# Kernel optimization log

Measured on AMD Instinct MI355X. Metric: run time of the kernel, lower is better.

The kernel has to match this reference:

```python
import jax, jax.numpy as jnp
import numpy as np

B, N, D = 8, 900, 256
SA_H, CA_H = 8, 8
L, P = 4, 4
FF = 2048
SHAPES = ((128, 128), (64, 64), (32, 32), (16, 16))
STARTS = (0, 16384, 20480, 21504)
S = 21760
D_BAND = (D // 6) * 2   # 84
D_ROPE = 3 * D_BAND     # 252
NF = D_BAND // 2        # 42
EPS = 1e-5


def _ln(x, g, b):
    mu = jnp.mean(x, -1, keepdims=True)
    var = jnp.mean((x - mu) ** 2, -1, keepdims=True)
    return (x - mu) * jax.lax.rsqrt(var + EPS) * g + b


def _rotate_half(x):
    x1 = x[..., 0::2]
    x2 = x[..., 1::2]
    return jnp.stack([-x2, x1], axis=-1).reshape(x.shape)


def _rope(q, k, boxes):
    freqs = 1.0 / (10000.0 ** (jnp.arange(NF, dtype=jnp.float32) / NF))
    cx, cy = boxes[..., 0], boxes[..., 1]
    xy = cx * cy

    def cs(v, f):
        a = v[..., None] * f
        return jnp.repeat(jnp.cos(a), 2, -1), jnp.repeat(jnp.sin(a), 2, -1)

    cx_c, cx_s = cs(cx, freqs)
    cy_c, cy_s = cs(cy, freqs)
    xy_c, xy_s = cs(xy, freqs * 0.1)
    cos = jnp.concatenate([cx_c, cy_c, xy_c], -1)
    sin = jnp.concatenate([cx_s, cy_s, xy_s], -1)

    def app(t):
        a, rest = t[..., :D_ROPE], t[..., D_ROPE:]
        return jnp.concatenate([a * cos + _rotate_half(a) * sin, rest], -1)

    return app(q), app(k)


def _bilinear(img, xy):
    # img: (Hl, Wl, C); xy: (M, 2) normalized in [0,1]
    # torch grid_sample semantics: align_corners=False, zero padding
    Hl, Wl, _ = img.shape
    x = xy[:, 0] * Wl - 0.5
    y = xy[:, 1] * Hl - 0.5
    x0 = jnp.floor(x)
    y0 = jnp.floor(y)
    lx = x - x0
    ly = y - y0
    x0i = x0.astype(jnp.int32)
    y0i = y0.astype(jnp.int32)

    def tap(yi, xi):
        valid = (xi >= 0) & (xi < Wl) & (yi >= 0) & (yi < Hl)
        v = img[jnp.clip(yi, 0, Hl - 1), jnp.clip(xi, 0, Wl - 1)]
        return v * valid[:, None].astype(v.dtype)

    return (tap(y0i, x0i) * ((1 - ly) * (1 - lx))[:, None]
            + tap(y0i, x0i + 1) * ((1 - ly) * lx)[:, None]
            + tap(y0i + 1, x0i) * (ly * (1 - lx))[:, None]
            + tap(y0i + 1, x0i + 1) * (ly * lx)[:, None])


def _forward(tgt, memory, query_pos, ref_boxes, reference_points,
             wq, bq, wk, bk, wv, bv, sa_wo, sa_bo, n1_g, n1_b,
             off_w, off_b, aw_w, aw_b, val_w, val_b, co_w, co_b,
             n2_g, n2_b, ff1_w, ff1_b, ff2_w, ff2_b, n3_g, n3_b):
    dh = D // SA_H
    # --- self attention with ComplexRoPE2D applied pre-projection ---
    q = tgt + query_pos
    k = tgt + query_pos
    q, k = _rope(q, k, ref_boxes)
    qh = (q @ wq + bq).reshape(B, N, SA_H, dh).transpose(0, 2, 1, 3)
    kh = (k @ wk + bk).reshape(B, N, SA_H, dh).transpose(0, 2, 1, 3)
    vh = (tgt @ wv + bv).reshape(B, N, SA_H, dh).transpose(0, 2, 1, 3)
    att = jax.nn.softmax(jnp.einsum('bhqd,bhkd->bhqk', qh, kh) * (dh ** -0.5), axis=-1)
    sa = jnp.einsum('bhqk,bhkd->bhqd', att, vh).transpose(0, 2, 1, 3).reshape(B, N, D)
    tgt = _ln(tgt + sa @ sa_wo + sa_bo, n1_g, n1_b)

    # --- multi-scale deformable cross-attention ---
    cdh = D // CA_H
    q2 = tgt + query_pos
    value = (memory @ val_w + val_b).reshape(B, S, CA_H, cdh)
    off = (q2 @ off_w + off_b).reshape(B, N, CA_H, L, P, 2)
    aw = jax.nn.softmax((q2 @ aw_w + aw_b).reshape(B, N, CA_H, L * P), axis=-1)
    aw = aw.reshape(B, N, CA_H, L, P)
    # offset normalizer is (W, H) per level
    normalizer = jnp.array([[w_, h_] for (h_, w_) in SHAPES], dtype=jnp.float32)
    loc = reference_points[:, :, None, :, None, :] + off / normalizer[None, None, None, :, None, :]
    out = jnp.zeros((B, CA_H, N, cdh), dtype=tgt.dtype)
    for l, (Hl, Wl) in enumerate(SHAPES):
        st = STARTS[l]
        v_l = value[:, st:st + Hl * Wl].reshape(B, Hl, Wl, CA_H, cdh)
        v_l = v_l.transpose(0, 3, 1, 2, 4).reshape(B * CA_H, Hl, Wl, cdh)
        loc_l = loc[:, :, :, l].transpose(0, 2, 1, 3, 4).reshape(B * CA_H, N * P, 2)
        s_l = jax.vmap(_bilinear)(v_l, loc_l).reshape(B, CA_H, N, P, cdh)
        out = out + jnp.einsum('bhnpd,bnhp->bhnd', s_l, aw[:, :, :, l])
    ca = out.transpose(0, 2, 1, 3).reshape(B, N, D) @ co_w + co_b
    tgt = _ln(tgt + ca, n2_g, n2_b)

    # --- FFN ---
    ff = jax.nn.relu(tgt @ ff1_w + ff1_b) @ ff2_w + ff2_b
    return _ln(tgt + ff, n3_g, n3_b)


def setup_inputs() -> dict:
    key = jax.random.key(0)
    ks = jax.random.split(key, 16)

    def wmat(k, shape):
        return jax.random.normal(k, shape, jnp.float32) * 0.02

    z = lambda *s: jnp.zeros(s, jnp.float32)
    o = lambda *s: jnp.ones(s, jnp.float32)
    return dict(
        tgt=jax.random.normal(ks[0], (B, N, D), jnp.float32),
        memory=jax.random.normal(ks[1], (B, S, D), jnp.float32),
        query_pos=jax.random.normal(ks[2], (B, N, D), jnp.float32) * 0.02,
        ref_boxes=jax.random.uniform(ks[3], (B, N, 4), jnp.float32),
        reference_points=jax.random.uniform(ks[4], (B, N, L, 2), jnp.float32),
        wq=wmat(ks[5], (D, D)), bq=z(D),
        wk=wmat(ks[6], (D, D)), bk=z(D),
        wv=wmat(ks[7], (D, D)), bv=z(D),
        sa_wo=wmat(ks[8], (D, D)), sa_bo=z(D),
        n1_g=o(D), n1_b=z(D),
        off_w=wmat(ks[9], (D, CA_H * L * P * 2)), off_b=z(CA_H * L * P * 2),
        aw_w=wmat(ks[10], (D, CA_H * L * P)), aw_b=z(CA_H * L * P),
        val_w=wmat(ks[11], (D, D)), val_b=z(D),
        co_w=wmat(ks[12], (D, D)), co_b=z(D),
        n2_g=o(D), n2_b=z(D),
        ff1_w=wmat(ks[13], (D, FF)), ff1_b=z(FF),
        ff2_w=wmat(ks[14], (FF, D)), ff2_b=z(D),
        n3_g=o(D), n3_b=z(D))


def reference(tgt, memory, query_pos, ref_boxes, reference_points,
              wq, bq, wk, bk, wv, bv, sa_wo, sa_bo, n1_g, n1_b,
              off_w, off_b, aw_w, aw_b, val_w, val_b, co_w, co_b,
              n2_g, n2_b, ff1_w, ff1_b, ff2_w, ff2_b, n3_g, n3_b):
    return _forward(tgt, memory, query_pos, ref_boxes, reference_points,
                    wq, bq, wk, bk, wv, bv, sa_wo, sa_bo, n1_g, n1_b,
                    off_w, off_b, aw_w, aw_b, val_w, val_b, co_w, co_b,
                    n2_g, n2_b, ff1_w, ff1_b, ff2_w, ff2_b, n3_g, n3_b)
```

## Files before the change

kernel.cpp:

```cpp
#include <hip/hip_runtime.h>
#include <hip/hip_bf16.h>
#include <math.h>

#define B_ 8
#define N_ 900
#define D_ 256
#define S_ 21760
#define H_ 8
#define DH 32
#define FF_ 2048
#define NROWS (B_*N_)

typedef __attribute__((ext_vector_type(8))) short bf16x8;
typedef __attribute__((ext_vector_type(4))) float f32x4;

union BU { bf16x8 v; short s[8]; unsigned long long u[2]; };

static __device__ inline short f2bf_s(float x) {
  __hip_bfloat16 h = __float2bfloat16(x);
  return *reinterpret_cast<short*>(&h);
}

__device__ __forceinline__ void gload_lds16(const float* g, float* lds) {
  __builtin_amdgcn_global_load_lds(
      (const __attribute__((address_space(1))) void*)g,
      (__attribute__((address_space(3))) void*)lds, 16, 0, 0);
}

__global__ __launch_bounds__(128) void rope_kernel(
    const float* __restrict__ tgt, const float* __restrict__ qpos,
    const float* __restrict__ boxes, __hip_bfloat16* __restrict__ out)
{
  int row = blockIdx.x;
  int tid = threadIdx.x;
  const float* x = tgt  + (size_t)row * D_;
  const float* p = qpos + (size_t)row * D_;
  float a0 = x[2*tid]   + p[2*tid];
  float a1 = x[2*tid+1] + p[2*tid+1];
  float o0 = a0, o1 = a1;
  if (tid < 126) {
    int band = tid / 42;
    int fi   = tid - band * 42;
    float freq = powf(10000.0f, -(float)fi / 42.0f);
    float cx = boxes[(size_t)row*4 + 0];
    float cy = boxes[(size_t)row*4 + 1];
    float v  = (band == 0) ? cx : (band == 1 ? cy : cx * cy);
    if (band == 2) freq *= 0.1f;
    float ang = v * freq;
    float c = cosf(ang), s = sinf(ang);
    o0 = a0 * c - a1 * s;
    o1 = a1 * c + a0 * s;
  }
  short2 sv = make_short2(f2bf_s(o0), f2bf_s(o1));
  *(short2*)&out[(size_t)row*D_ + 2*tid] = sv;
}

__global__ __launch_bounds__(256) void wtrans_kernel(
    const float* __restrict__ wq, const float* __restrict__ wk,
    const float* __restrict__ wv, const float* __restrict__ sa_wo,
    const float* __restrict__ offw, const float* __restrict__ valw,
    const float* __restrict__ cow, const float* __restrict__ aww,
    const float* __restrict__ ff1w, const float* __restrict__ ff2w,
    short* __restrict__ Wt)
{
  int bid = blockIdx.x;
  const float* W; short* out; int K, N, tile;
  if (bid < 448) {
    int wi = bid >> 6; tile = bid & 63; K = 256; N = 256;
    const float* tab[7] = {wq, wk, wv, sa_wo, offw, valw, cow};
    const int   off[7]  = {0, 65536, 131072, 196608, 262144, 360448, 425984};
    W = tab[wi]; out = Wt + off[wi];
  } else if (bid < 480) {
    tile = bid - 448; K = 256; N = 128; W = aww; out = Wt + 327680;
  } else if (bid < 992) {
    tile = bid - 480; K = 256; N = 2048; W = ff1w; out = Wt + 491520;
  } else {
    tile = bid - 992; K = 2048; N = 256; W = ff2w; out = Wt + 1015808;
  }
  int ntn = N >> 5;
  int tk = tile / ntn, tn = tile - tk * ntn;
  __shared__ float t[32][33];
  int c = threadIdx.x & 31, rr = threadIdx.x >> 5;
  #pragma unroll
  for (int i = 0; i < 4; ++i)
    t[rr + i*8][c] = W[(size_t)(tk*32 + rr + i*8) * N + tn*32 + c];
  __syncthreads();
  #pragma unroll
  for (int i = 0; i < 4; ++i)
    out[(size_t)(tn*32 + rr + i*8) * K + tk*32 + c] = f2bf_s(t[c][rr + i*8]);
}

template<int BM, int KK, bool ABF16, bool A2ADD, bool RELU, int OUTMODE>
__global__ __launch_bounds__(256) void mgemm_kernel(
    const void* __restrict__ Ap, const float* __restrict__ A2p,
    const short* __restrict__ Wt,
    const float* __restrict__ bias, const float* __restrict__ bias2,
    void* __restrict__ Cp, void* __restrict__ Cp2, int M, int N,
    const float* __restrict__ Xres, const float* __restrict__ lng,
    const float* __restrict__ lnb)
{
  constexpr int MS = BM / 16;
  constexpr bool SWAP = (OUTMODE != 2);
  __shared__ short As[BM * 256];
  int tid = threadIdx.x;
  int w = tid >> 6, lane = tid & 63;
  int g = lane >> 4, r = lane & 15;
  int m0 = blockIdx.x * BM;
  int nw = blockIdx.y * 256 + w * 64;
  bool active = nw < N;

  f32x4 acc[MS][4];
  #pragma unroll
  for (int i = 0; i < MS; ++i)
    #pragma unroll
    for (int j = 0; j < 4; ++j) acc[i][j] = (f32x4){0.f,0.f,0.f,0.f};

  for (int kb = 0; kb < KK; kb += 256) {
    if (KK > 256 && kb) __syncthreads();
    #pragma unroll
    for (int i = 0; i < BM/8; ++i) {
      int u = i*256 + tid;
      int row = u >> 5, c8 = u & 31;
      BU pk;
      if (ABF16) {
        pk.v = *(const bf16x8*)((const short*)Ap + (size_t)(m0+row)*KK + kb + c8*8);
      } else {
        const float* ap = (const float*)Ap + (size_t)(m0+row)*KK + kb + c8*8;
        float4 a0 = *(const float4*)ap;
        float4 a1 = *(const float4*)(ap + 4);
        if (A2ADD) {
          const float* a2 = A2p + (size_t)(m0+row)*KK + kb + c8*8;
          float4 b0 = *(const float4*)a2;
          float4 b1 = *(const float4*)(a2 + 4);
          a0.x += b0.x; a0.y += b0.y; a0.z += b0.z; a0.w += b0.w;
          a1.x += b1.x; a1.y += b1.y; a1.z += b1.z; a1.w += b1.w;
        }
        pk.s[0]=f2bf_s(a0.x); pk.s[1]=f2bf_s(a0.y); pk.s[2]=f2bf_s(a0.z); pk.s[3]=f2bf_s(a0.w);
        pk.s[4]=f2bf_s(a1.x); pk.s[5]=f2bf_s(a1.y); pk.s[6]=f2bf_s(a1.z); pk.s[7]=f2bf_s(a1.w);
      }
      int col = (c8*8) ^ ((row & 7) << 3);
      *(bf16x8*)&As[row*256 + col] = pk.v;
    }
    __syncthreads();
    if (active) {
      #pragma unroll
      for (int kk = 0; kk < 8; ++kk) {
        BU bfr[4];
        #pragma unroll
        for (int ns = 0; ns < 4; ++ns) {
          const short* wp = Wt + (size_t)(nw + ns*16 + r)*KK + kb + kk*32;
          bfr[ns].u[0] = *(const unsigned long long*)(wp + 4*g);
          bfr[ns].u[1] = *(const unsigned long long*)(wp + 16 + 4*g);
        }
        #pragma unroll
        for (int ms = 0; ms < MS; ++ms) {
          int row = ms*16 + r;
          int c0 = (kk*32 + g*4)      ^ ((r & 7) << 3);
          int c1 = (kk*32 + 16 + g*4) ^ ((r & 7) << 3);
          BU af;
          af.u[0] = *(const unsigned long long*)&As[row*256 + c0];
          af.u[1] = *(const unsigned long long*)&As[row*256 + c1];
          #pragma unroll
          for (int ns = 0; ns < 4; ++ns) {
            if (SWAP)
              acc[ms][ns] = __builtin_amdgcn_mfma_f32_16x16x32_bf16(
                  bfr[ns].v, af.v, acc[ms][ns], 0, 0, 0);
            else
              acc[ms][ns] = __builtin_amdgcn_mfma_f32_16x16x32_bf16(
                  af.v, bfr[ns].v, acc[ms][ns], 0, 0, 0);
          }
        }
      }
    }
  }

  if (OUTMODE == 5) {
    float vv[MS][16];
    float ps[MS], pq[MS];
    #pragma unroll
    for (int ms = 0; ms < MS; ++ms) {
      ps[ms] = 0.f; pq[ms] = 0.f;
      int m = m0 + ms*16 + r;
      #pragma unroll
      for (int ns = 0; ns < 4; ++ns) {
        int n0 = nw + ns*16 + g*4;
        float4 b4 = *(const float4*)&bias[n0];
        float4 x4 = *(const float4*)&Xres[(size_t)m*256 + n0];
        #pragma unroll
        for (int j = 0; j < 4; ++j) {
          float v = acc[ms][ns][j] + ((const float*)&b4)[j] + ((const float*)&x4)[j];
          vv[ms][ns*4 + j] = v;
          ps[ms] += v; pq[ms] += v*v;
        }
      }
      ps[ms] += __shfl_xor(ps[ms], 16); ps[ms] += __shfl_xor(ps[ms], 32);
      pq[ms] += __shfl_xor(pq[ms], 16); pq[ms] += __shfl_xor(pq[ms], 32);
    }
    __syncthreads();
    float* red = (float*)As;
    if (g == 0) {
      #pragma unroll
      for (int ms = 0; ms < MS; ++ms) {
        red[(ms*16 + r)*8 + w]     = ps[ms];
        red[(ms*16 + r)*8 + 4 + w] = pq[ms];
      }
    }
    __syncthreads();
    #pragma unroll
    for (int ms = 0; ms < MS; ++ms) {
      int rowi = ms*16 + r;
      float ts = red[rowi*8+0]+red[rowi*8+1]+red[rowi*8+2]+red[rowi*8+3];
      float tq = red[rowi*8+4]+red[rowi*8+5]+red[rowi*8+6]+red[rowi*8+7];
      float mu = ts * (1.0f/256.0f);
      float var = tq * (1.0f/256.0f) - mu*mu;
      float rs = rsqrtf(fmaxf(var, 0.f) + 1e-5f);
      int m = m0 + ms*16 + r;
      #pragma unroll
      for (int ns = 0; ns < 4; ++ns) {
        int n0 = nw + ns*16 + g*4;
        float4 g4 = *(const float4*)&lng[n0];
        float4 be = *(const float4*)&lnb[n0];
        float4 ov;
        ov.x = (vv[ms][ns*4+0] - mu)*rs*g4.x + be.x;
        ov.y = (vv[ms][ns*4+1] - mu)*rs*g4.y + be.y;
        ov.z = (vv[ms][ns*4+2] - mu)*rs*g4.z + be.z;
        ov.w = (vv[ms][ns*4+3] - mu)*rs*g4.w + be.w;
        *(float4*)&((float*)Cp)[(size_t)m*256 + n0] = ov;
      }
    }
    return;
  }

  if (!active) return;

  #pragma unroll
  for (int ms = 0; ms < MS; ++ms) {
    #pragma unroll
    for (int ns = 0; ns < 4; ++ns) {
      if (SWAP) {
        int n0 = nw + ns*16 + g*4;
        int m  = m0 + ms*16 + r;
        float4 b4;
        if (OUTMODE == 3 || OUTMODE == 4)
          b4 = (n0 < 256) ? *(const float4*)&bias[n0]
                          : *(const float4*)&bias2[n0 - 256];
        else
          b4 = *(const float4*)&bias[n0];
        float v0 = acc[ms][ns][0] + b4.x;
        float v1 = acc[ms][ns][1] + b4.y;
        float v2 = acc[ms][ns][2] + b4.z;
        float v3 = acc[ms][ns][3] + b4.w;
        if (RELU) {
          v0 = fmaxf(v0, 0.f); v1 = fmaxf(v1, 0.f);
          v2 = fmaxf(v2, 0.f); v3 = fmaxf(v3, 0.f);
        }
        if (OUTMODE == 0) {
          *(float4*)&((float*)Cp)[(size_t)m*N + n0] = make_float4(v0,v1,v2,v3);
        } else if (OUTMODE == 1) {
          short4 sv = make_short4(f2bf_s(v0), f2bf_s(v1), f2bf_s(v2), f2bf_s(v3));
          *(short4*)&((short*)Cp)[(size_t)m*N + n0] = sv;
        } else if (OUTMODE == 3) {
          short4 sv = make_short4(f2bf_s(v0), f2bf_s(v1), f2bf_s(v2), f2bf_s(v3));
          if (n0 < 256) *(short4*)&((short*)Cp )[(size_t)m*256 + n0]       = sv;
          else          *(short4*)&((short*)Cp2)[(size_t)m*256 + (n0-256)] = sv;
        } else {
          float4 fv = make_float4(v0,v1,v2,v3);
          if (n0 < 256) *(float4*)&((float*)Cp )[(size_t)m*256 + n0]       = fv;
          else          *(float4*)&((float*)Cp2)[(size_t)m*128 + (n0-256)] = fv;
        }
      } else {
        int n = nw + ns*16 + r;
        float bsc = bias[n];
        int hh = n >> 5, dd = n & 31;
        int mb = m0 + ms*16 + g*4;
        short4 sv = make_short4(
            f2bf_s(acc[ms][ns][0] + bsc), f2bf_s(acc[ms][ns][1] + bsc),
            f2bf_s(acc[ms][ns][2] + bsc), f2bf_s(acc[ms][ns][3] + bsc));
        int bb = mb / N_, bbe = (mb + 3) / N_;
        if (bb == bbe) {
          int nn = mb - bb * N_;
          *(short4*)&((short*)Cp)[((size_t)((bb*H_ + hh)*DH + dd))*N_ + nn] = sv;
        } else {
          const short* sp = (const short*)&sv;
          #pragma unroll
          for (int j = 0; j < 4; ++j) {
            int m = mb + j;
            int b2 = m / N_, nn = m - b2 * N_;
            ((short*)Cp)[((size_t)((b2*H_ + hh)*DH + dd))*N_ + nn] = sp[j];
          }
        }
      }
    }
  }
}

__global__ __launch_bounds__(512) void vgemm_kernel(
    const float* __restrict__ Ap, const short* __restrict__ Wt,
    const float* __restrict__ bias, short* __restrict__ Cp)
{
  __shared__ float buf[8][1024];
  __shared__ float dump[1024];
  int tid = threadIdx.x;
  int w = tid >> 6, l = tid & 63;
  int g = l >> 4, r = l & 15;
  int nw = w * 32;

  BU wreg[2][8];
  #pragma unroll
  for (int ns = 0; ns < 2; ++ns) {
    const short* wp = Wt + (size_t)(nw + ns*16 + r) * 256;
    #pragma unroll
    for (int kk = 0; kk < 8; ++kk) {
      wreg[ns][kk].u[0] = *(const unsigned long long*)(wp + kk*32 + 4*g);
      wreg[ns][kk].u[1] = *(const unsigned long long*)(wp + kk*32 + 16 + 4*g);
    }
  }
  float4 bs4[2];
  #pragma unroll
  for (int ns = 0; ns < 2; ++ns) bs4[ns] = *(const float4*)&bias[nw + ns*16 + g*4];

  bool stager = (w < 4);
  int srow = (w & 3)*8 + (l >> 3);
  int schunk = (l & 7) ^ (srow & 7);
  const float* gbase = Ap + ((size_t)blockIdx.x*160 + srow) * 256 + schunk*4;

  if (stager) {
    #pragma unroll
    for (int t = 0; t < 6; ++t)
      gload_lds16(gbase + (t>>3)*8192 + (t&7)*32, &buf[t][(w & 3)*256]);
  }

  f32x4 acc[2][2];
  #pragma unroll
  for (int i = 0; i < 2; ++i)
    #pragma unroll
    for (int j = 0; j < 2; ++j) acc[i][j] = (f32x4){0.f,0.f,0.f,0.f};

  int bb = blockIdx.x / 136;
  int pixblk = (blockIdx.x % 136) * 160;

  for (int s = 0; s < 5; ++s) {
    #pragma unroll
    for (int c = 0; c < 8; ++c) {
      int t = s*8 + c;
      int tn = t + 6;
      if (stager) {
        if (tn < 40) gload_lds16(gbase + (tn>>3)*8192 + (tn&7)*32,
                                 &buf[(c+6)&7][(w & 3)*256]);
        else         gload_lds16(gbase, &dump[(w & 3)*256]);
        asm volatile("s_waitcnt vmcnt(6)" ::: "memory");
      }
      __builtin_amdgcn_s_barrier();
      const float* bp = &buf[c][0];
      #pragma unroll
      for (int ms = 0; ms < 2; ++ms) {
        int row = ms*16 + r;
        const float* rp = bp + row*32;
        float4 f0 = *(const float4*)&rp[((g    ) ^ (row & 7)) * 4];
        float4 f1 = *(const float4*)&rp[((g + 4) ^ (row & 7)) * 4];
        BU af;
        af.s[0]=f2bf_s(f0.x); af.s[1]=f2bf_s(f0.y); af.s[2]=f2bf_s(f0.z); af.s[3]=f2bf_s(f0.w);
        af.s[4]=f2bf_s(f1.x); af.s[5]=f2bf_s(f1.y); af.s[6]=f2bf_s(f1.z); af.s[7]=f2bf_s(f1.w);
        #pragma unroll
        for (int ns = 0; ns < 2; ++ns)
          acc[ms][ns] = __builtin_amdgcn_mfma_f32_16x16x32_bf16(
              wreg[ns][c].v, af.v, acc[ms][ns], 0, 0, 0);
      }
    }
    int pix0 = pixblk + s*32;
    #pragma unroll
    for (int ms = 0; ms < 2; ++ms) {
      #pragma unroll
      for (int ns = 0; ns < 2; ++ns) {
        int pix = pix0 + ms*16 + r;
        int n0  = nw + ns*16 + g*4;
        int hh = n0 >> 5, dd = n0 & 31;
        short4 sv = make_short4(
            f2bf_s(acc[ms][ns][0] + bs4[ns].x),
            f2bf_s(acc[ms][ns][1] + bs4[ns].y),
            f2bf_s(acc[ms][ns][2] + bs4[ns].z),
            f2bf_s(acc[ms][ns][3] + bs4[ns].w));
        *(short4*)&Cp[((size_t)(bb*H_ + hh)*S_ + pix)*32 + dd] = sv;
        acc[ms][ns] = (f32x4){0.f,0.f,0.f,0.f};
      }
    }
  }
}

__global__ __launch_bounds__(64) void mfma_attn_kernel(
    const __hip_bfloat16* __restrict__ Q,
    const __hip_bfloat16* __restrict__ K,
    const __hip_bfloat16* __restrict__ Vt,
    __hip_bfloat16* __restrict__ O)
{
  const int NQT = 29;
  int wid = blockIdx.x;
  int qt = wid % NQT, bh = wid / NQT;
  int b = bh >> 3, h = bh & 7;
  int lane = threadIdx.x;
  int g = lane >> 4, r = lane & 15;
  int q0 = qt * 32;
  const float scale = 0.17677669529663687f;

  union U { bf16x8 v; short s[8]; unsigned long long u64[2]; };

  U qf[2];
  #pragma unroll
  for (int qq = 0; qq < 2; ++qq) {
    int qrow = min(q0 + qq*16 + r, N_ - 1);
    const __hip_bfloat16* qp = Q + ((size_t)(b*N_ + qrow))*D_ + h*DH;
    qf[qq].u64[0] = *(const unsigned long long*)(qp + 4*g);
    qf[qq].u64[1] = *(const unsigned long long*)(qp + 16 + 4*g);
  }

  f32x4 oaccA[2], oaccB[2];
  #pragma unroll
  for (int qq = 0; qq < 2; ++qq) {
    oaccA[qq] = (f32x4){0.f,0.f,0.f,0.f};
    oaccB[qq] = (f32x4){0.f,0.f,0.f,0.f};
  }
  float m0v = -1e30f, m1v = -1e30f, l0v = 0.f, l1v = 0.f;
  const f32x4 zero = {0.f,0.f,0.f,0.f};

  const __hip_bfloat16* vbase0 = Vt + (size_t)(bh*DH + r) * N_;
  const __hip_bfloat16* vbase1 = Vt + (size_t)(bh*DH + 16 + r) * N_;

  for (int kt = 0; kt < N_; kt += 32) {
    U kf0, kf1;
    {
      int kr0 = min(kt + r, N_ - 1);
      int kr1 = min(kt + 16 + r, N_ - 1);
      const __hip_bfloat16* kp0 = K + ((size_t)(b*N_ + kr0))*D_ + h*DH;
      const __hip_bfloat16* kp1 = K + ((size_t)(b*N_ + kr1))*D_ + h*DH;
      kf0.u64[0] = *(const unsigned long long*)(kp0 + 4*g);
      kf0.u64[1] = *(const unsigned long long*)(kp0 + 16 + 4*g);
      kf1.u64[0] = *(const unsigned long long*)(kp1 + 4*g);
      kf1.u64[1] = *(const unsigned long long*)(kp1 + 16 + 4*g);
    }
    U vf0, vf1;
    vf0.u64[0] = *(const unsigned long long*)(vbase0 + kt + 4*g);
    vf0.u64[1] = *(const unsigned long long*)(vbase0 + kt + 16 + 4*g);
    vf1.u64[0] = *(const unsigned long long*)(vbase1 + kt + 4*g);
    vf1.u64[1] = *(const unsigned long long*)(vbase1 + kt + 16 + 4*g);

    #pragma unroll
    for (int qq = 0; qq < 2; ++qq) {
      f32x4 s0 = __builtin_amdgcn_mfma_f32_16x16x32_bf16(kf0.v, qf[qq].v, zero, 0, 0, 0);
      f32x4 s1 = __builtin_amdgcn_mfma_f32_16x16x32_bf16(kf1.v, qf[qq].v, zero, 0, 0, 0);
      float m = qq ? m1v : m0v;
      float lv = qq ? l1v : l0v;

      float sc[8];
      #pragma unroll
      for (int j = 0; j < 4; ++j) {
        sc[j]   = (kt + 4*g + j      < N_) ? s0[j] * scale : -1e30f;
        sc[4+j] = (kt + 16 + 4*g + j < N_) ? s1[j] * scale : -1e30f;
      }
      float mx = sc[0];
      #pragma unroll
      for (int j = 1; j < 8; ++j) mx = fmaxf(mx, sc[j]);
      mx = fmaxf(mx, __shfl_xor(mx, 16));
      mx = fmaxf(mx, __shfl_xor(mx, 32));

      float mnew = fmaxf(m, mx);
      float corr = __expf(m - mnew);
      float p[8], ps = 0.f;
      #pragma unroll
      for (int j = 0; j < 8; ++j) { p[j] = __expf(sc[j] - mnew); ps += p[j]; }
      ps += __shfl_xor(ps, 16);
      ps += __shfl_xor(ps, 32);
      lv = lv * corr + ps;
      if (qq) { m1v = mnew; l1v = lv; } else { m0v = mnew; l0v = lv; }
      #pragma unroll
      for (int j = 0; j < 4; ++j) { oaccA[qq][j] *= corr; oaccB[qq][j] *= corr; }

      U pf;
      #pragma unroll
      for (int j = 0; j < 8; ++j) pf.s[j] = f2bf_s(p[j]);

      oaccA[qq] = __builtin_amdgcn_mfma_f32_16x16x32_bf16(vf0.v, pf.v, oaccA[qq], 0, 0, 0);
      oaccB[qq] = __builtin_amdgcn_mfma_f32_16x16x32_bf16(vf1.v, pf.v, oaccB[qq], 0, 0, 0);
    }
  }

  #pragma unroll
  for (int qq = 0; qq < 2; ++qq) {
    int qrow = q0 + qq*16 + r;
    if (qrow < N_) {
      float inv = 1.0f / (qq ? l1v : l0v);
      short* op = (short*)(O + ((size_t)(b*N_ + qrow))*D_ + h*DH);
      short4 sA = make_short4(
          f2bf_s(oaccA[qq][0]*inv), f2bf_s(oaccA[qq][1]*inv),
          f2bf_s(oaccA[qq][2]*inv), f2bf_s(oaccA[qq][3]*inv));
      short4 sB = make_short4(
          f2bf_s(oaccB[qq][0]*inv), f2bf_s(oaccB[qq][1]*inv),
          f2bf_s(oaccB[qq][2]*inv), f2bf_s(oaccB[qq][3]*inv));
      *(short4*)&op[4*g]      = sA;
      *(short4*)&op[16 + 4*g] = sB;
    }
  }
}

__global__ __launch_bounds__(256) void sample4_kernel(
    const __hip_bfloat16* __restrict__ V, const float* __restrict__ offp,
    const float* __restrict__ awl, const float* __restrict__ refp,
    short* __restrict__ out)
{
  int tid = threadIdx.x;
  int q = tid >> 6, t = tid & 63;
  int row = blockIdx.x * 4 + q;
  int b = row / N_;
  __shared__ float s_aw[4][128];
  __shared__ float s_loc[4][256];
  #pragma unroll
  for (int i = 0; i < 2; ++i)
    s_aw[q][t + i*64] = awl[(size_t)row*128 + t + i*64];
  {
    const float norms[4] = {128.f, 64.f, 32.f, 16.f};
    #pragma unroll
    for (int i = 0; i < 4; ++i) {
      int e = t + i*64;
      int rem = e & 31, li = rem >> 3, ax = rem & 1;
      s_loc[q][e] = refp[((size_t)row*4 + li)*2 + ax]
                  + offp[(size_t)row*256 + e] / norms[li];
    }
  }
  __syncthreads();
  if (t < 8) {
    float mx = -1e30f;
    for (int j = 0; j < 16; ++j) mx = fmaxf(mx, s_aw[q][t*16+j]);
    float sum = 0.f;
    for (int j = 0; j < 16; ++j) sum += __expf(s_aw[q][t*16+j] - mx);
    float inv = 1.0f / sum;
    for (int j = 0; j < 16; ++j)
      s_aw[q][t*16+j] = __expf(s_aw[q][t*16+j] - mx) * inv;
  }
  __syncthreads();
  int h = t >> 3, dq = t & 7;
  const int dims[4]   = {128, 64, 32, 16};
  const int starts[4] = {0, 16384, 20480, 21504};
  const __hip_bfloat16* Vb = V + ((size_t)(b*H_ + h) * S_) * 32 + dq*4;
  float a0 = 0.f, a1 = 0.f, a2 = 0.f, a3 = 0.f;
  #pragma unroll
  for (int l = 0; l < 4; ++l) {
    int Wl = dims[l], st = starts[l];
    #pragma unroll
    for (int p = 0; p < 4; ++p) {
      float lx = s_loc[q][h*32 + l*8 + p*2 + 0];
      float ly = s_loc[q][h*32 + l*8 + p*2 + 1];
      float x = lx * Wl - 0.5f, y = ly * Wl - 0.5f;
      float x0f = floorf(x), y0f = floorf(y);
      float fx = x - x0f, fy = y - y0f;
      int x0 = (int)x0f, y0 = (int)y0f;
      float v0 = 0.f, v1 = 0.f, v2 = 0.f, v3 = 0.f;
      #pragma unroll
      for (int ty = 0; ty < 2; ++ty) {
        int yi = y0 + ty;
        float wy = ty ? fy : (1.f - fy);
        if (yi < 0 || yi >= Wl) continue;
        #pragma unroll
        for (int txi = 0; txi < 2; ++txi) {
          int xi = x0 + txi;
          float wx = txi ? fx : (1.f - fx);
          if (xi < 0 || xi >= Wl) continue;
          unsigned long long vv =
              *(const unsigned long long*)&Vb[(size_t)(st + yi*Wl + xi) * 32];
          float ww = wy * wx;
          v0 += ww * __uint_as_float((unsigned)(vv) << 16);
          v1 += ww * __uint_as_float((unsigned)(vv) & 0xffff0000u);
          v2 += ww * __uint_as_float((unsigned)(vv >> 32) << 16);
          v3 += ww * __uint_as_float((unsigned)(vv >> 32) & 0xffff0000u);
        }
      }
      float aw = s_aw[q][h*16 + l*4 + p];
      a0 += aw * v0; a1 += aw * v1; a2 += aw * v2; a3 += aw * v3;
    }
  }
  short4 sv = make_short4(f2bf_s(a0), f2bf_s(a1), f2bf_s(a2), f2bf_s(a3));
  *(short4*)&out[(size_t)row*D_ + h*DH + dq*4] = sv;
}

extern "C" void kernel_launch(void* const* d_in, const int* in_sizes, int n_in,
                              void* d_out, int out_size, void* d_ws, size_t ws_size,
                              hipStream_t stream)
{
  const float* tgt    = (const float*)d_in[0];
  const float* memory = (const float*)d_in[1];
  const float* qpos   = (const float*)d_in[2];
  const float* boxes  = (const float*)d_in[3];
  const float* refp   = (const float*)d_in[4];
  const float* wq = (const float*)d_in[5];   const float* bq = (const float*)d_in[6];
  const float* wk = (const float*)d_in[7];   const float* bk = (const float*)d_in[8];
  const float* wv = (const float*)d_in[9];   const float* bv = (const float*)d_in[10];
  const float* sa_wo = (const float*)d_in[11]; const float* sa_bo = (const float*)d_in[12];
  const float* n1g = (const float*)d_in[13]; const float* n1b = (const float*)d_in[14];
  const float* off_w = (const float*)d_in[15]; const float* off_b = (const float*)d_in[16];
  const float* aw_w  = (const float*)d_in[17]; const float* aw_b  = (const float*)d_in[18];
  const float* val_w = (const float*)d_in[19]; const float* val_b = (const float*)d_in[20];
  const float* co_w  = (const float*)d_in[21]; const float* co_b  = (const float*)d_in[22];
  const float* n2g = (const float*)d_in[23]; const float* n2b = (const float*)d_in[24];
  const float* ff1_w = (const float*)d_in[25]; const float* ff1_b = (const float*)d_in[26];
  const float* ff2_w = (const float*)d_in[27]; const float* ff2_b = (const float*)d_in[28];
  const float* n3g = (const float*)d_in[29]; const float* n3b = (const float*)d_in[30];

  char* ws = (char*)d_ws;
  size_t NE = (size_t)NROWS * D_;
  __hip_bfloat16* Vv = (__hip_bfloat16*)ws;
  __hip_bfloat16* FFM = (__hip_bfloat16*)ws;
  size_t p = (size_t)B_ * S_ * D_ * sizeof(__hip_bfloat16);
  float* A  = (float*)(ws + p); p += NE*4;
  float* Qb = (float*)(ws + p); p += NE*4;
  float* Kb = (float*)(ws + p); p += NE*4;
  float* Vh = (float*)(ws + p); p += NE*4;
  float* S1 = (float*)(ws + p); p += NE*4;
  float* S2 = (float*)(ws + p); p += NE*4;
  float* T1 = (float*)(ws + p); p += NE*4;
  short* Wt = (short*)((char*)Kb + NE*2);
  float* out = (float*)d_out;
  (void)ws_size; (void)in_sizes; (void)n_in; (void)out_size; (void)S2;

  const short* qk_t  = Wt;
  const short* wv_t  = Wt + 131072;
  const short* sa_t  = Wt + 196608;
  const short* offaw_t = Wt + 262144;
  const short* val_t = Wt + 360448;
  const short* co_t  = Wt + 425984;
  const short* ff1_t = Wt + 491520;
  const short* ff2_t = Wt + 1015808;

  wtrans_kernel<<<1504, 256, 0, stream>>>(wq, wk, wv, sa_wo, off_w, val_w,
                                          co_w, aw_w, ff1_w, ff2_w, Wt);

  rope_kernel<<<NROWS, 128, 0, stream>>>(tgt, qpos, boxes, (__hip_bfloat16*)A);
  mgemm_kernel<32,256,true,false,false,3><<<dim3(225,2), 256, 0, stream>>>(
      A, nullptr, qk_t, bq, bk, Qb, Kb, NROWS, 512, nullptr, nullptr, nullptr);
  mgemm_kernel<32,256,false,false,false,2><<<dim3(225,1), 256, 0, stream>>>(
      tgt, nullptr, wv_t, bv, nullptr, Vh, nullptr, NROWS, 256, nullptr, nullptr, nullptr);
  mfma_attn_kernel<<<29 * B_ * H_, 64, 0, stream>>>(
      (const __hip_bfloat16*)Qb, (const __hip_bfloat16*)Kb,
      (const __hip_bfloat16*)Vh, (__hip_bfloat16*)S1);
  mgemm_kernel<32,256,true,false,false,5><<<dim3(225,1), 256, 0, stream>>>(
      S1, nullptr, sa_t, sa_bo, nullptr, T1, nullptr, NROWS, 256, tgt, n1g, n1b);

  vgemm_kernel<<<1088, 512, 0, stream>>>(memory, val_t, val_b, (short*)Vv);
  mgemm_kernel<32,256,false,true,false,4><<<dim3(225,2), 256, 0, stream>>>(
      T1, qpos, offaw_t, off_b, aw_b, Qb, Kb, NROWS, 384, nullptr, nullptr, nullptr);
  sample4_kernel<<<NROWS/4, 256, 0, stream>>>(Vv, Qb, Kb, refp, (short*)S1);
  mgemm_kernel<32,256,true,false,false,5><<<dim3(225,1), 256, 0, stream>>>(
      S1, nullptr, co_t, co_b, nullptr, T1, nullptr, NROWS, 256, T1, n2g, n2b);

  mgemm_kernel<32,256,false,false,true,1><<<dim3(225,8), 256, 0, stream>>>(
      T1, nullptr, ff1_t, ff1_b, nullptr, FFM, nullptr, NROWS, FF_, nullptr, nullptr, nullptr);
  mgemm_kernel<32,2048,true,false,false,5><<<dim3(225,1), 256, 0, stream>>>(
      FFM, nullptr, ff2_t, ff2_b, nullptr, out, nullptr, NROWS, 256, T1, n3g, n3b);
}
```

Measured before the change: 412.8 us.

## Fuse FFN up and down projections into one kernel keeping hidden tile on-chip

Replaces the two separate FFN GEMM launches with a single kernel that processes 16 rows per block, computing each 256-wide hidden chunk with ReLU into LDS and immediately accumulating it into the second projection, then applying residual and LayerNorm. This removes the global write and read of the large bf16 hidden activation buffer and one kernel launch. In exchange each small block streams the full weight matrices directly from global memory without LDS staging, lowering weight reuse and potentially becoming L2-bandwidth or latency bound.

```diff
diff --git a/kernel.cpp b/kernel.cpp
--- a/kernel.cpp
+++ b/kernel.cpp
@@ -294,6 +294,139 @@
   }
 }
 
+__global__ __launch_bounds__(256) void ffn_kernel(
+    const float* __restrict__ T1, const short* __restrict__ W1t,
+    const float* __restrict__ b1, const short* __restrict__ W2t,
+    const float* __restrict__ b2, const float* __restrict__ lng,
+    const float* __restrict__ lnb, float* __restrict__ out)
+{
+  __shared__ short As[16*256];
+  __shared__ short Hs[16*256];
+  int tid = threadIdx.x;
+  int w = tid >> 6, lane = tid & 63;
+  int g = lane >> 4, r = lane & 15;
+  int m0 = blockIdx.x * 16;
+  int nw = w * 64;
+
+  #pragma unroll
+  for (int i = 0; i < 2; ++i) {
+    int u = i*256 + tid;
+    int row = u >> 5, c8 = u & 31;
+    const float* ap = T1 + (size_t)(m0+row)*256 + c8*8;
+    float4 a0 = *(const float4*)ap;
+    float4 a1 = *(const float4*)(ap + 4);
+    BU pk;
+    pk.s[0]=f2bf_s(a0.x); pk.s[1]=f2bf_s(a0.y); pk.s[2]=f2bf_s(a0.z); pk.s[3]=f2bf_s(a0.w);
+    pk.s[4]=f2bf_s(a1.x); pk.s[5]=f2bf_s(a1.y); pk.s[6]=f2bf_s(a1.z); pk.s[7]=f2bf_s(a1.w);
+    int col = (c8*8) ^ ((row & 7) << 3);
+    *(bf16x8*)&As[row*256 + col] = pk.v;
+  }
+  __syncthreads();
+
+  f32x4 acc2[4];
+  #pragma unroll
+  for (int ns = 0; ns < 4; ++ns) acc2[ns] = (f32x4){0.f,0.f,0.f,0.f};
+
+  for (int h = 0; h < 8; ++h) {
+    f32x4 acc1[4];
+    #pragma unroll
+    for (int ns = 0; ns < 4; ++ns) acc1[ns] = (f32x4){0.f,0.f,0.f,0.f};
+    #pragma unroll
+    for (int kk = 0; kk < 8; ++kk) {
+      BU bfr[4];
+      #pragma unroll
+      for (int ns = 0; ns < 4; ++ns) {
+        const short* wp = W1t + (size_t)(h*256 + nw + ns*16 + r)*256 + kk*32;
+        bfr[ns].u[0] = *(const unsigned long long*)(wp + 4*g);
+        bfr[ns].u[1] = *(const unsigned long long*)(wp + 16 + 4*g);
+      }
+      int c0 = (kk*32 + g*4)      ^ ((r & 7) << 3);
+      int c1 = (kk*32 + 16 + g*4) ^ ((r & 7) << 3);
+      BU af;
+      af.u[0] = *(const unsigned long long*)&As[r*256 + c0];
+      af.u[1] = *(const unsigned long long*)&As[r*256 + c1];
+      #pragma unroll
+      for (int ns = 0; ns < 4; ++ns)
+        acc1[ns] = __builtin_amdgcn_mfma_f32_16x16x32_bf16(
+            bfr[ns].v, af.v, acc1[ns], 0, 0, 0);
+    }
+    __syncthreads();
+    #pragma unroll
+    for (int ns = 0; ns < 4; ++ns) {
+      int n0c = nw + ns*16 + g*4;
+      float4 bb4 = *(const float4*)&b1[h*256 + n0c];
+      short4 sv = make_short4(
+          f2bf_s(fmaxf(acc1[ns][0] + bb4.x, 0.f)),
+          f2bf_s(fmaxf(acc1[ns][1] + bb4.y, 0.f)),
+          f2bf_s(fmaxf(acc1[ns][2] + bb4.z, 0.f)),
+          f2bf_s(fmaxf(acc1[ns][3] + bb4.w, 0.f)));
+      *(short4*)&Hs[r*256 + (n0c ^ ((r & 7) << 3))] = sv;
+    }
+    __syncthreads();
+    #pragma unroll
+    for (int kk = 0; kk < 8; ++kk) {
+      BU bfr[4];
+      #pragma unroll
+      for (int ns = 0; ns < 4; ++ns) {
+        const short* wp = W2t + (size_t)(nw + ns*16 + r)*2048 + h*256 + kk*32;
+        bfr[ns].u[0] = *(const unsigned long long*)(wp + 4*g);
+        bfr[ns].u[1] = *(const unsigned long long*)(wp + 16 + 4*g);
+      }
+      int c0 = (kk*32 + g*4)      ^ ((r & 7) << 3);
+      int c1 = (kk*32 + 16 + g*4) ^ ((r & 7) << 3);
+      BU af;
+      af.u[0] = *(const unsigned long long*)&Hs[r*256 + c0];
+      af.u[1] = *(const unsigned long long*)&Hs[r*256 + c1];
+      #pragma unroll
+      for (int ns = 0; ns < 4; ++ns)
+        acc2[ns] = __builtin_amdgcn_mfma_f32_16x16x32_bf16(
+            bfr[ns].v, af.v, acc2[ns], 0, 0, 0);
+    }
+  }
+
+  float vv[16];
+  float ps = 0.f, pq = 0.f;
+  int m = m0 + r;
+  #pragma unroll
+  for (int ns = 0; ns < 4; ++ns) {
+    int n0 = nw + ns*16 + g*4;
+    float4 b4 = *(const float4*)&b2[n0];
+    float4 x4 = *(const float4*)&T1[(size_t)m*256 + n0];
+    #pragma unroll
+    for (int j = 0; j < 4; ++j) {
+      float v = acc2[ns][j] + ((const float*)&b4)[j] + ((const float*)&x4)[j];
+      vv[ns*4 + j] = v;
+      ps += v; pq += v*v;
+    }
+  }
+  ps += __shfl_xor(ps, 16); ps += __shfl_xor(ps, 32);
+  pq += __shfl_xor(pq, 16); pq += __shfl_xor(pq, 32);
+  __syncthreads();
+  float* red = (float*)Hs;
+  if (g == 0) {
+    red[r*8 + w]     = ps;
+    red[r*8 + 4 + w] = pq;
+  }
+  __syncthreads();
+  float ts = red[r*8+0]+red[r*8+1]+red[r*8+2]+red[r*8+3];
+  float tq = red[r*8+4]+red[r*8+5]+red[r*8+6]+red[r*8+7];
+  float mu = ts * (1.0f/256.0f);
+  float var = tq * (1.0f/256.0f) - mu*mu;
+  float rs = rsqrtf(fmaxf(var, 0.f) + 1e-5f);
+  #pragma unroll
+  for (int ns = 0; ns < 4; ++ns) {
+    int n0 = nw + ns*16 + g*4;
+    float4 g4 = *(const float4*)&lng[n0];
+    float4 be = *(const float4*)&lnb[n0];
+    float4 ov;
+    ov.x = (vv[ns*4+0] - mu)*rs*g4.x + be.x;
+    ov.y = (vv[ns*4+1] - mu)*rs*g4.y + be.y;
+    ov.z = (vv[ns*4+2] - mu)*rs*g4.z + be.z;
+    ov.w = (vv[ns*4+3] - mu)*rs*g4.w + be.w;
+    *(float4*)&out[(size_t)m*256 + n0] = ov;
+  }
+}
+
 __global__ __launch_bounds__(512) void vgemm_kernel(
     const float* __restrict__ Ap, const short* __restrict__ Wt,
     const float* __restrict__ bias, short* __restrict__ Cp)
@@ -606,7 +739,6 @@
   char* ws = (char*)d_ws;
   size_t NE = (size_t)NROWS * D_;
   __hip_bfloat16* Vv = (__hip_bfloat16*)ws;
-  __hip_bfloat16* FFM = (__hip_bfloat16*)ws;
   size_t p = (size_t)B_ * S_ * D_ * sizeof(__hip_bfloat16);
   float* A  = (float*)(ws + p); p += NE*4;
   float* Qb = (float*)(ws + p); p += NE*4;
@@ -649,8 +781,6 @@
   mgemm_kernel<32,256,true,false,false,5><<<dim3(225,1), 256, 0, stream>>>(
       S1, nullptr, co_t, co_b, nullptr, T1, nullptr, NROWS, 256, T1, n2g, n2b);
 
-  mgemm_kernel<32,256,false,false,true,1><<<dim3(225,8), 256, 0, stream>>>(
-      T1, nullptr, ff1_t, ff1_b, nullptr, FFM, nullptr, NROWS, FF_, nullptr, nullptr, nullptr);
-  mgemm_kernel<32,2048,true,false,false,5><<<dim3(225,1), 256, 0, stream>>>(
-      FFM, nullptr, ff2_t, ff2_b, nullptr, out, nullptr, NROWS, 256, T1, n3g, n3b);
-}
+  ffn_kernel<<<450, 256, 0, stream>>>(T1, ff1_t, ff1_b, ff2_t, ff2_b,
+                                      n3g, n3b, out);
+}
```

After: 509.6 us. +23.4%, slower.
